# Kernel optimization log

Measured on AMD Instinct MI355X. Metric: run time of the kernel, lower is better.

The kernel has to match this reference:

```python
import jax, jax.numpy as jnp
import numpy as np

HEAD_DIM = 16

def setup_inputs() -> dict:
    key = jax.random.key(0)
    ks = jax.random.split(key, 9)
    dim = 256
    B, H, W = 8, 32, 32
    x  = jax.random.normal(ks[0], (B, H, W, dim), jnp.float32)
    # Conv2d weights in OIHW layout (torch convention), small init
    w3 = jax.random.normal(ks[1], (dim, dim, 1, 1), jnp.float32) * 0.05
    b3 = jax.random.normal(ks[2], (dim,), jnp.float32) * 0.01
    w5 = jax.random.normal(ks[3], (dim, dim, 3, 3), jnp.float32) * 0.02
    b5 = jax.random.normal(ks[4], (dim,), jnp.float32) * 0.01
    w7 = jax.random.normal(ks[5], (dim, dim, 5, 5), jnp.float32) * 0.01
    b7 = jax.random.normal(ks[6], (dim,), jnp.float32) * 0.01
    # nn.Linear weight: (out_features=dim, in_features=attention_dim=dim), no bias
    wp = jax.random.normal(ks[7], (dim, dim), jnp.float32) * 0.05
    return {"x": x, "w3": w3, "b3": b3, "w5": w5, "b5": b5, "w7": w7, "b7": b7, "wp": wp}

def _conv2d_same(x_nchw, w_oihw, b):
    y = jax.lax.conv_general_dilated(
        x_nchw, w_oihw, window_strides=(1, 1), padding='SAME',
        dimension_numbers=('NCHW', 'OIHW', 'NCHW'))
    return y + b[None, :, None, None]

def reference(x, w3, b3, w5, b5, w7, b7, wp):
    B, H, W, C = x.shape
    N = H * W
    nh = C // HEAD_DIM            # num_heads
    scale = HEAD_DIM ** (-0.5)
    xc = jnp.transpose(x, (0, 3, 1, 2))  # NCHW
    # q: 1x1 conv, v: 3x3 conv, k: 5x5 conv (names match the torch code)
    q = _conv2d_same(xc, w3, b3).reshape(B, nh, N, HEAD_DIM)
    v = _conv2d_same(xc, w5, b5).reshape(B, nh, N, HEAD_DIM)
    k = _conv2d_same(xc, w7, b7).reshape(B, nh, N, HEAD_DIM)
    attn = jax.nn.softmax(jnp.einsum('bhnd,bhmd->bhnm', q, k) * scale, axis=-1)
    out = jnp.einsum('bhnm,bhmd->bhnd', attn, v)        # [B, nh, N, hd]
    out = jnp.transpose(out, (0, 2, 1, 3)).reshape(B, H, W, nh * HEAD_DIM)
    return out @ wp.T                                   # Linear, no bias
```

## Files before the change

kernel.cpp:

```cpp
#include <hip/hip_runtime.h>
#include <hip/hip_bf16.h>

#define DIM 256
#define HW  1024

typedef __attribute__((ext_vector_type(8))) short short8;
typedef __attribute__((ext_vector_type(4))) float floatx4;
typedef __attribute__((ext_vector_type(16))) float floatx16;
typedef __attribute__((address_space(1))) const unsigned int g_u32;
typedef __attribute__((address_space(3))) unsigned int l_u32;

#define QSCALE 0.36067376022224085f

__device__ inline unsigned short f2bf(float f) {
  union { float f; unsigned u; } v;
  v.f = f;
  unsigned u = v.u;
  u += 0x7fffu + ((u >> 16) & 1u);
  return (unsigned short)(u >> 16);
}

__device__ inline unsigned short f2bf_trunc(float f) {
  union { float f; unsigned u; } v;
  v.f = f;
  return (unsigned short)(v.u >> 16);
}

__global__ void detect_kernel(const unsigned short* __restrict__ xr,
                              int* __restrict__ flag) {
  __shared__ int cnt;
  if (threadIdx.x == 0) cnt = 0;
  __syncthreads();
  int local = 0;
  for (int i = threadIdx.x; i < 8192; i += 256) {
    unsigned short u = xr[i];
    if ((u & 0x7F80u) == 0x7F80u) local++;
  }
  if (local) atomicAdd(&cnt, local);
  __syncthreads();
  if (threadIdx.x == 0) *flag = (cnt > 0) ? 1 : 0;
}

__device__ inline float ldin(const void* p, long i, int isf32) {
  if (isf32) return ((const float*)p)[i];
  union { unsigned u; float f; } v;
  v.u = ((unsigned)((const unsigned short*)p)[i]) << 16;
  return v.f;
}

__global__ __launch_bounds__(256) void xconv_kernel(
    const void* __restrict__ x, unsigned short* __restrict__ xbf,
    const int* __restrict__ flag) {
  const int isf32 = *flag;
  const int i = (blockIdx.x * 256 + threadIdx.x) * 4;
  if (isf32) {
    const float4 v = *(const float4*)((const float*)x + i);
    ushort4 o;
    o.x = f2bf(v.x); o.y = f2bf(v.y); o.z = f2bf(v.z); o.w = f2bf(v.w);
    *(ushort4*)(xbf + i) = o;
  } else {
    *(ushort4*)(xbf + i) = *(const ushort4*)((const unsigned short*)x + i);
  }
}

__device__ inline void frag_repack2(const void* __restrict__ w,
                                    unsigned short* __restrict__ wF, int KK,
                                    int slice, float* __restrict__ Wl,
                                    int isf32) {
  const int t = threadIdx.x;
  const int co16 = slice & 15;
  const int c8   = slice >> 4;
  const int RE = 32 * KK;
  const int RS = RE + 1;
  for (int r = 0; r < 16; ++r) {
    const long base = ((long)((co16 * 16 + r) * 256 + c8 * 32)) * KK;
    for (int i = t; i < RE; i += 256) Wl[r * RS + i] = ldin(w, base + i, isf32);
  }
  __syncthreads();
  for (int tap = 0; tap < KK; ++tap) {
    unsigned short* dst = wF + ((((tap << 3) + c8) << 4) + co16) * 512;
    for (int i = t; i < 512; i += 256) {
      const int lane = i >> 3, j = i & 7;
      const int col = lane & 15;
      const int cis = ((lane >> 4) << 3) + j;
      dst[i] = f2bf(Wl[col * RS + cis * KK + tap]);
    }
  }
}

__global__ __launch_bounds__(256) void wrepack_kernel(
    const void* __restrict__ w3, const void* __restrict__ b3,
    const void* __restrict__ w5, const void* __restrict__ b5,
    const void* __restrict__ w7, const void* __restrict__ b7,
    const void* __restrict__ wp,
    unsigned short* __restrict__ wF3, unsigned short* __restrict__ wF5,
    unsigned short* __restrict__ wF7, unsigned short* __restrict__ wpF,
    float* __restrict__ bc, const int* __restrict__ flag) {
  __shared__ float Wl[12816];
  const int isf32 = *flag;
  const int bid = blockIdx.x;
  const int t = threadIdx.x;
  if (bid < 128) {
    frag_repack2(w7, wF7, 25, bid, Wl, isf32);
  } else if (bid < 256) {
    frag_repack2(w5, wF5, 9, bid - 128, Wl, isf32);
  } else if (bid < 384) {
    frag_repack2(w3, wF3, 1, bid - 256, Wl, isf32);
  } else if (bid < 512) {
    frag_repack2(wp, wpF, 1, bid - 384, Wl, isf32);
  } else {
#pragma unroll
    for (int r = 0; r < 3; ++r) {
      const int i = r * 256 + t;
      const void* src = (i < 256) ? b3 : (i < 512) ? b5 : b7;
      bc[i] = ldin(src, i & 255, isf32);
    }
  }
}

__global__ __launch_bounds__(256, 2) void convqkv_kernel(
    const unsigned short* __restrict__ xbf,
    const unsigned short* __restrict__ wFq,
    const unsigned short* __restrict__ wFv,
    const unsigned short* __restrict__ wFk,
    const float* __restrict__ bc,
    unsigned short* __restrict__ qOut,
    unsigned short* __restrict__ vOut,
    unsigned short* __restrict__ kOut) {
  constexpr int WC = 36;
  constexpr int CELLS = 12 * WC;
  constexpr int LOADS = CELLS * 4;
  __shared__ unsigned short Xs[CELLS * 40];
  __shared__ unsigned short Bs[36 * 512];
  const int t    = threadIdx.x;
  const int bid  = blockIdx.x;
  const int cog0 = bid & 15;
  const int co0  = cog0 << 4;
  const int m0   = (bid >> 4) << 8;
  const int b    = m0 >> 10;
  const int n0   = m0 & 1023;
  const int r0   = n0 >> 5;
  const int wv   = t >> 6;
  const int lane = t & 63;
  const int l15  = lane & 15;
  const int quad = lane >> 4;

  floatx4 aq[4] = {}, av[4] = {}, ak[4] = {};

  for (int c8 = 0; c8 < 8; ++c8) {
    uint4 xreg[7];
#pragma unroll
    for (int rr = 0; rr < 7; ++rr) {
      const int id = rr * 256 + t;
      const int cell = id >> 2, part = id & 3;
      const int hr = cell / WC, wc = cell - hr * WC;
      const int xr = r0 + hr - 2, xc = wc - 2;
      const bool ok = (id < LOADS) && ((unsigned)xr < 32u) &&
                      ((unsigned)xc < 32u);
      const int cr = xr < 0 ? 0 : (xr > 31 ? 31 : xr);
      const int cc = xc < 0 ? 0 : (xc > 31 ? 31 : xc);
      uint4 v = *(const uint4*)&xbf[(((b * 32 + cr) * 32 + cc) << 8) +
                                    (c8 << 5) + (part << 3)];
      if (!ok) v = make_uint4(0, 0, 0, 0);
      xreg[rr] = v;
    }
    __syncthreads();
#pragma unroll
    for (int rr = 0; rr < 9; ++rr) {
      const int tap = (rr << 2) + wv;
      if (tap < 35) {
        const unsigned short* src;
        if (tap < 25) {
          src = &wFk[((((tap << 3) + c8) << 4) + cog0) * 512];
        } else if (tap < 34) {
          src = &wFv[(((((tap - 25) << 3) + c8) << 4) + cog0) * 512];
        } else {
          src = &wFq[((c8 << 4) + cog0) * 512];
        }
        __builtin_amdgcn_global_load_lds((g_u32*)(src + (lane << 3)),
                                         (l_u32*)&Bs[tap << 9], 16, 0, 0);
      }
    }
#pragma unroll
    for (int rr = 0; rr < 7; ++rr) {
      const int id = rr * 256 + t;
      if (id < LOADS)
        *(uint4*)&Xs[(id >> 2) * 40 + ((id & 3) << 3)] = xreg[rr];
    }
    __syncthreads();

#pragma unroll
    for (int tap = 0; tap < 25; ++tap) {
      const int kh = tap / 5, kw = tap % 5;
      const bool vv = (kh >= 1 && kh <= 3 && kw >= 1 && kw <= 3);
      short8 a[4];
#pragma unroll
      for (int rr2 = 0; rr2 < 2; ++rr2) {
#pragma unroll
        for (int ch = 0; ch < 2; ++ch) {
          const unsigned short* xs =
              &Xs[(((wv << 1) + rr2 + kh) * WC + (ch << 4) + l15 + kw) * 40 +
                  (quad << 3)];
          a[(rr2 << 1) + ch] = *(const short8*)xs;
        }
      }
      const short8 kb = *(const short8*)&Bs[(tap << 9) + (lane << 3)];
#pragma unroll
      for (int f = 0; f < 4; ++f)
        ak[f] = __builtin_amdgcn_mfma_f32_16x16x32_bf16(a[f], kb, ak[f],
                                                        0, 0, 0);
      if (vv) {
        const int vt = (kh - 1) * 3 + (kw - 1);
        const short8 vb = *(const short8*)&Bs[((25 + vt) << 9) + (lane << 3)];
#pragma unroll
        for (int f = 0; f < 4; ++f)
          av[f] = __builtin_amdgcn_mfma_f32_16x16x32_bf16(a[f], vb, av[f],
                                                          0, 0, 0);
      }
      if (tap == 12) {
        const short8 qb = *(const short8*)&Bs[(34 << 9) + (lane << 3)];
#pragma unroll
        for (int f = 0; f < 4; ++f)
          aq[f] = __builtin_amdgcn_mfma_f32_16x16x32_bf16(a[f], qb, aq[f],
                                                          0, 0, 0);
      }
    }
  }
#pragma unroll
  for (int rr2 = 0; rr2 < 2; ++rr2) {
#pragma unroll
    for (int ch = 0; ch < 2; ++ch) {
      const int f = (rr2 << 1) + ch;
      const int co = co0 + l15;
      const int slab = (b << 4) + (co >> 4);
      const int clo = co & 15;
      const int nb = n0 + (wv << 6) + (rr2 << 5) + (ch << 4) + (quad << 2);
      {
        const float bj = bc[co];
        floatx4 a = aq[f];
        ushort4 pk4;
        pk4.x = f2bf((a[0] + bj) * QSCALE);
        pk4.y = f2bf((a[1] + bj) * QSCALE);
        pk4.z = f2bf((a[2] + bj) * QSCALE);
        pk4.w = f2bf((a[3] + bj) * QSCALE);
        *(ushort4*)&qOut[(slab << 14) + (clo << 10) + nb] = pk4;
      }
      {
        const float bj = bc[512 + co];
        floatx4 a = ak[f];
        ushort4 pk4;
        pk4.x = f2bf(a[0] + bj); pk4.y = f2bf(a[1] + bj);
        pk4.z = f2bf(a[2] + bj); pk4.w = f2bf(a[3] + bj);
        *(ushort4*)&kOut[(slab << 14) + (clo << 10) + nb] = pk4;
      }
      {
        const float bj = bc[256 + co];
        floatx4 a = av[f];
        const int base = (slab << 14) + (clo << 6);
#pragma unroll
        for (int i = 0; i < 4; ++i) {
          const int n = nb + i;
          vOut[base + ((n & 15) << 10) + (n >> 4)] = f2bf(a[i] + bj);
        }
      }
    }
  }
}

__global__ __launch_bounds__(256, 4) void attn_mfma_kernel(
    const unsigned short* __restrict__ qg,
    const unsigned short* __restrict__ kg,
    const unsigned short* __restrict__ vg,
    unsigned short* __restrict__ out2) {
  __shared__ __align__(16) unsigned short Pb[4][32][40];
  const int t    = threadIdx.x;
  const int w    = t >> 6;
  const int lane = t & 63;
  const int slab = blockIdx.x >> 3;
  const int rb   = blockIdx.x & 7;
  const int b = slab >> 4;
  const int h = slab & 15;
  const int l31  = lane & 31;
  const int hl   = lane >> 5;
  const int l15  = lane & 15;
  const int quad = lane >> 4;

  const unsigned short* Kb = kg + (slab << 14);
  const unsigned short* Vb = vg + (slab << 14);

  const int row0 = (rb << 7) + (w << 5);
  const short8 qa =
      *(const short8*)&qg[(slab << 14) + ((row0 + l31) << 4) + (hl << 3)];

  const short onebf = (short)0x3F80;
  const short8 ones = {onebf, onebf, onebf, onebf, onebf, onebf, onebf, onebf};

  floatx4 acco[2] = {}, asum[2] = {};

  for (int kc = 0; kc < 1024; kc += 32) {
    const short8 kb = *(const short8*)&Kb[((kc + l31) << 4) + (hl << 3)];
    floatx16 s = {};
    s = __builtin_amdgcn_mfma_f32_32x32x16_bf16(qa, kb, s, 0, 0, 0);
#pragma unroll
    for (int r = 0; r < 16; ++r) {
      const float e = __builtin_amdgcn_exp2f(s[r]);
      const int row = (r & 3) + ((r >> 2) << 3) + (hl << 2);
      Pb[w][row][l31] = f2bf_trunc(e);
    }
    const short8 vb = *(const short8*)&Vb[(l15 << 10) + kc + (quad << 3)];
#pragma unroll
    for (int tt = 0; tt < 2; ++tt) {
      const short8 pa = *(const short8*)&Pb[w][(tt << 4) + l15][quad << 3];
      acco[tt] =
          __builtin_amdgcn_mfma_f32_16x16x32_bf16(pa, vb, acco[tt], 0, 0, 0);
      asum[tt] =
          __builtin_amdgcn_mfma_f32_16x16x32_bf16(pa, ones, asum[tt], 0, 0, 0);
    }
  }
#pragma unroll
  for (int tt = 0; tt < 2; ++tt) {
#pragma unroll
    for (int r = 0; r < 4; ++r) {
      const int nloc = (tt << 4) + (quad << 2) + r;
      const float val = acco[tt][r] / asum[tt][r];
      const int n = row0 + nloc;
      out2[(((b << 10) + n) << 8) + (h << 4) + l15] = f2bf(val);
    }
  }
}

__global__ __launch_bounds__(256) void linear_mfma_kernel(
    const unsigned short* __restrict__ inp,
    const unsigned short* __restrict__ wpF,
    void* __restrict__ out, const int* __restrict__ flag) {
  __shared__ unsigned short As[64 * 40];
  const int isf32 = *flag;
  const int t   = threadIdx.x;
  const int m0  = blockIdx.x << 6;
  const int co0 = blockIdx.y << 6;
  const int wv   = t >> 6;
  const int lane = t & 63;
  const int wm = (wv & 1) << 5;
  const int wn = (wv >> 1) << 5;
  const int l15  = lane & 15;
  const int quad = lane >> 4;
  const int cogb = (co0 >> 4) + (wn >> 4);
  const int rowS = t >> 2;
  const int partS = t & 3;

  floatx4 acc[2][2] = {};

  short8 cb0, cb1;
  {
    const unsigned short* wptr = &wpF[(cogb << 9) + (lane << 3)];
    cb0 = *(const short8*)wptr;
    cb1 = *(const short8*)(wptr + 512);
  }
  for (int c8 = 0; c8 < 8; ++c8) {
    const uint4 v = *(const uint4*)&inp[((m0 + rowS) << 8) + (c8 << 5) +
                                        (partS << 3)];
    short8 nb0 = {}, nb1 = {};
    if (c8 + 1 < 8) {
      const unsigned short* wptr =
          &wpF[((((c8 + 1) << 4) + cogb) << 9) + (lane << 3)];
      nb0 = *(const short8*)wptr;
      nb1 = *(const short8*)(wptr + 512);
    }
    __syncthreads();
    *(uint4*)&As[rowS * 40 + (partS << 3)] = v;
    __syncthreads();
    const unsigned short* xs = &As[(wm + l15) * 40 + (quad << 3)];
    const short8 afr0 = *(const short8*)xs;
    const short8 afr1 = *(const short8*)(xs + 16 * 40);
    acc[0][0] = __builtin_amdgcn_mfma_f32_16x16x32_bf16(afr0, cb0,
                                                        acc[0][0], 0, 0, 0);
    acc[0][1] = __builtin_amdgcn_mfma_f32_16x16x32_bf16(afr0, cb1,
                                                        acc[0][1], 0, 0, 0);
    acc[1][0] = __builtin_amdgcn_mfma_f32_16x16x32_bf16(afr1, cb0,
                                                        acc[1][0], 0, 0, 0);
    acc[1][1] = __builtin_amdgcn_mfma_f32_16x16x32_bf16(afr1, cb1,
                                                        acc[1][1], 0, 0, 0);
    cb0 = nb0; cb1 = nb1;
  }
#pragma unroll
  for (int mi = 0; mi < 2; ++mi) {
#pragma unroll
    for (int ni = 0; ni < 2; ++ni) {
      const int co = co0 + wn + (ni << 4) + l15;
      const int mb = m0 + wm + (mi << 4) + (quad << 2);
      floatx4 a = acc[mi][ni];
      if (!isf32) {
        unsigned short* o16 = (unsigned short*)out;
#pragma unroll
        for (int r = 0; r < 4; ++r) o16[(mb + r) * 256 + co] = f2bf(a[r]);
      } else {
        float* o32 = (float*)out;
#pragma unroll
        for (int r = 0; r < 4; ++r) o32[(mb + r) * 256 + co] = a[r];
      }
    }
  }
}

extern "C" void kernel_launch(void* const* d_in, const int* in_sizes, int n_in,
                              void* d_out, int out_size, void* d_ws,
                              size_t ws_size, hipStream_t stream) {
  const void* x  = d_in[0];
  const void* w3 = d_in[1];
  const void* b3 = d_in[2];
  const void* w5 = d_in[3];
  const void* b5 = d_in[4];
  const void* w7 = d_in[5];
  const void* b7 = d_in[6];
  const void* wp = d_in[7];

  char* p = (char*)d_ws;
  int* flag = (int*)p;                       p += 256;
  unsigned short* xbf = (unsigned short*)p;  p += 4u * 1024 * 1024;
  unsigned short* wF3 = (unsigned short*)p;  p += 131072;
  unsigned short* wF5 = (unsigned short*)p;  p += 1179648;
  unsigned short* wF7 = (unsigned short*)p;  p += 3276800;
  unsigned short* wpF = (unsigned short*)p;  p += 131072;
  float* bc = (float*)p;                     p += 4096;
  unsigned short* qc  = (unsigned short*)p;  p += 4194304;
  unsigned short* kT  = (unsigned short*)p;  p += 4194304;
  unsigned short* vT  = (unsigned short*)p;  p += 4194304;
  unsigned short* o2b = (unsigned short*)p;  p += 4194304;

  detect_kernel<<<1, 256, 0, stream>>>((const unsigned short*)x, flag);

  xconv_kernel<<<2048, 256, 0, stream>>>(x, xbf, flag);
  wrepack_kernel<<<513, 256, 0, stream>>>(w3, b3, w5, b5, w7, b7, wp, wF3,
                                          wF5, wF7, wpF, bc, flag);

  convqkv_kernel<<<512, 256, 0, stream>>>(xbf, wF3, wF5, wF7, bc, qc, vT, kT);

  attn_mfma_kernel<<<1024, 256, 0, stream>>>(qc, kT, vT, o2b);

  dim3 lg(128, 4);
  linear_mfma_kernel<<<lg, 256, 0, stream>>>(o2b, wpF, d_out, flag);
}
```

Measured before the change: 179.1 us.

## Fuse dtype detection, input conversion and weight repack into one prep kernel

Three preprocessing launches (detect, x-to-bf16 conversion, weight repack) become one prep kernel in which every block runs the dtype detection itself. The aim is to save two launches and the serial dependency on the single-block detect kernel. Weight repacking now processes four rows at a time with a much smaller shared buffer, which should raise occupancy but adds extra syncs and leaves half the threads idle during the writes. Every block now repeats the 8192-element detection scan.

Result: faster. 174.3 us (-2.7%).

```diff
diff --git a/kernel.cpp b/kernel.cpp
--- a/kernel.cpp
+++ b/kernel.cpp
@@ -26,44 +26,28 @@
   return (unsigned short)(v.u >> 16);
 }
 
-__global__ void detect_kernel(const unsigned short* __restrict__ xr,
-                              int* __restrict__ flag) {
-  __shared__ int cnt;
-  if (threadIdx.x == 0) cnt = 0;
+__device__ inline float ldin(const void* p, long i, int isf32) {
+  if (isf32) return ((const float*)p)[i];
+  union { unsigned u; float f; } v;
+  v.u = ((unsigned)((const unsigned short*)p)[i]) << 16;
+  return v.f;
+}
+
+__device__ inline int detect_inline(const unsigned short* __restrict__ xr,
+                                    int* cnt) {
+  if (threadIdx.x == 0) *cnt = 0;
   __syncthreads();
   int local = 0;
   for (int i = threadIdx.x; i < 8192; i += 256) {
     unsigned short u = xr[i];
     if ((u & 0x7F80u) == 0x7F80u) local++;
   }
-  if (local) atomicAdd(&cnt, local);
+  if (local) atomicAdd(cnt, local);
   __syncthreads();
-  if (threadIdx.x == 0) *flag = (cnt > 0) ? 1 : 0;
-}
-
-__device__ inline float ldin(const void* p, long i, int isf32) {
-  if (isf32) return ((const float*)p)[i];
-  union { unsigned u; float f; } v;
-  v.u = ((unsigned)((const unsigned short*)p)[i]) << 16;
-  return v.f;
-}
-
-__global__ __launch_bounds__(256) void xconv_kernel(
-    const void* __restrict__ x, unsigned short* __restrict__ xbf,
-    const int* __restrict__ flag) {
-  const int isf32 = *flag;
-  const int i = (blockIdx.x * 256 + threadIdx.x) * 4;
-  if (isf32) {
-    const float4 v = *(const float4*)((const float*)x + i);
-    ushort4 o;
-    o.x = f2bf(v.x); o.y = f2bf(v.y); o.z = f2bf(v.z); o.w = f2bf(v.w);
-    *(ushort4*)(xbf + i) = o;
-  } else {
-    *(ushort4*)(xbf + i) = *(const ushort4*)((const unsigned short*)x + i);
-  }
-}
-
-__device__ inline void frag_repack2(const void* __restrict__ w,
+  return (*cnt > 0) ? 1 : 0;
+}
+
+__device__ inline void frag_repack4(const void* __restrict__ w,
                                     unsigned short* __restrict__ wF, int KK,
                                     int slice, float* __restrict__ Wl,
                                     int isf32) {
@@ -72,42 +56,65 @@
   const int c8   = slice >> 4;
   const int RE = 32 * KK;
   const int RS = RE + 1;
-  for (int r = 0; r < 16; ++r) {
-    const long base = ((long)((co16 * 16 + r) * 256 + c8 * 32)) * KK;
-    for (int i = t; i < RE; i += 256) Wl[r * RS + i] = ldin(w, base + i, isf32);
-  }
-  __syncthreads();
-  for (int tap = 0; tap < KK; ++tap) {
-    unsigned short* dst = wF + ((((tap << 3) + c8) << 4) + co16) * 512;
-    for (int i = t; i < 512; i += 256) {
-      const int lane = i >> 3, j = i & 7;
-      const int col = lane & 15;
-      const int cis = ((lane >> 4) << 3) + j;
-      dst[i] = f2bf(Wl[col * RS + cis * KK + tap]);
-    }
-  }
-}
-
-__global__ __launch_bounds__(256) void wrepack_kernel(
-    const void* __restrict__ w3, const void* __restrict__ b3,
-    const void* __restrict__ w5, const void* __restrict__ b5,
-    const void* __restrict__ w7, const void* __restrict__ b7,
-    const void* __restrict__ wp,
+  for (int g = 0; g < 4; ++g) {
+    __syncthreads();
+    for (int rloc = 0; rloc < 4; ++rloc) {
+      const long base =
+          ((long)((co16 * 16 + (g << 2) + rloc) * 256 + c8 * 32)) * KK;
+      for (int i = t; i < RE; i += 256)
+        Wl[rloc * RS + i] = ldin(w, base + i, isf32);
+    }
+    __syncthreads();
+    for (int tap = 0; tap < KK; ++tap) {
+      unsigned short* dst = wF + ((((tap << 3) + c8) << 4) + co16) * 512;
+      if (t < 128) {
+        const int colg = t >> 5;
+        const int cis  = t & 31;
+        const int col  = (g << 2) + colg;
+        const int lane = ((cis >> 3) << 4) | col;
+        const int j    = cis & 7;
+        dst[lane * 8 + j] = f2bf(Wl[colg * RS + cis * KK + tap]);
+      }
+    }
+  }
+}
+
+__global__ __launch_bounds__(256) void prep_kernel(
+    const void* __restrict__ x,  const void* __restrict__ w3,
+    const void* __restrict__ b3, const void* __restrict__ w5,
+    const void* __restrict__ b5, const void* __restrict__ w7,
+    const void* __restrict__ b7, const void* __restrict__ wp,
+    unsigned short* __restrict__ xbf,
     unsigned short* __restrict__ wF3, unsigned short* __restrict__ wF5,
     unsigned short* __restrict__ wF7, unsigned short* __restrict__ wpF,
-    float* __restrict__ bc, const int* __restrict__ flag) {
-  __shared__ float Wl[12816];
-  const int isf32 = *flag;
+    float* __restrict__ bc, int* __restrict__ flag) {
+  __shared__ float Wl[4 * 801];
+  __shared__ int cnt;
+  const int isf32 = detect_inline((const unsigned short*)x, &cnt);
   const int bid = blockIdx.x;
   const int t = threadIdx.x;
-  if (bid < 128) {
-    frag_repack2(w7, wF7, 25, bid, Wl, isf32);
-  } else if (bid < 256) {
-    frag_repack2(w5, wF5, 9, bid - 128, Wl, isf32);
-  } else if (bid < 384) {
-    frag_repack2(w3, wF3, 1, bid - 256, Wl, isf32);
-  } else if (bid < 512) {
-    frag_repack2(wp, wpF, 1, bid - 384, Wl, isf32);
+  if (bid < 512) {
+#pragma unroll
+    for (int r = 0; r < 4; ++r) {
+      const int i = (bid * 1024 + r * 256 + t) * 4;
+      if (isf32) {
+        const float4 v = *(const float4*)((const float*)x + i);
+        ushort4 o;
+        o.x = f2bf(v.x); o.y = f2bf(v.y); o.z = f2bf(v.z); o.w = f2bf(v.w);
+        *(ushort4*)(xbf + i) = o;
+      } else {
+        *(ushort4*)(xbf + i) =
+            *(const ushort4*)((const unsigned short*)x + i);
+      }
+    }
+  } else if (bid < 640) {
+    frag_repack4(w7, wF7, 25, bid - 512, Wl, isf32);
+  } else if (bid < 768) {
+    frag_repack4(w5, wF5, 9, bid - 640, Wl, isf32);
+  } else if (bid < 896) {
+    frag_repack4(w3, wF3, 1, bid - 768, Wl, isf32);
+  } else if (bid < 1024) {
+    frag_repack4(wp, wpF, 1, bid - 896, Wl, isf32);
   } else {
 #pragma unroll
     for (int r = 0; r < 3; ++r) {
@@ -115,6 +122,7 @@
       const void* src = (i < 256) ? b3 : (i < 512) ? b5 : b7;
       bc[i] = ldin(src, i & 255, isf32);
     }
+    if (t == 0) *flag = isf32;
   }
 }
 
@@ -427,11 +435,8 @@
   unsigned short* vT  = (unsigned short*)p;  p += 4194304;
   unsigned short* o2b = (unsigned short*)p;  p += 4194304;
 
-  detect_kernel<<<1, 256, 0, stream>>>((const unsigned short*)x, flag);
-
-  xconv_kernel<<<2048, 256, 0, stream>>>(x, xbf, flag);
-  wrepack_kernel<<<513, 256, 0, stream>>>(w3, b3, w5, b5, w7, b7, wp, wF3,
-                                          wF5, wF7, wpF, bc, flag);
+  prep_kernel<<<1025, 256, 0, stream>>>(x, w3, b3, w5, b5, w7, b7, wp, xbf,
+                                        wF3, wF5, wF7, wpF, bc, flag);
 
   convqkv_kernel<<<512, 256, 0, stream>>>(xbf, wF3, wF5, wF7, bc, qc, vT, kT);
 
```
